# Kernel optimization log

Hardware: AMD Instinct MI355X
Metric: run time of the kernel (lower is better)

## Reference

```python
import jax, jax.numpy as jnp
import numpy as np

B, S, DIM, BITS, HEXPERTS = 4, 4096, 2048, 32, 4


def setup_inputs() -> dict:
    key = jax.random.key(0)
    ks = jax.random.split(key, 6)
    scale = 1.0 / np.sqrt(DIM)
    return {
        "x": jax.random.normal(ks[0], (B, S, DIM), dtype=jnp.float32),
        "A1_w": jax.random.normal(ks[1], (BITS, DIM), dtype=jnp.float32) * scale,
        "A1_b": jax.random.normal(ks[2], (BITS,), dtype=jnp.float32) * 0.01,
        "emb": jax.random.normal(ks[3], (BITS, DIM), dtype=jnp.float32),
        "aggr_w": jax.random.normal(ks[4], (HEXPERTS,), dtype=jnp.float32) * 0.5,
        "aggr_b": jax.random.normal(ks[5], (1,), dtype=jnp.float32) * 0.01,
    }


def reference(x, A1_w, A1_b, emb, aggr_w, aggr_b):
    # Router: small linear [B,S,DIM] -> [B,S,BITS], softmax over bits.
    logits = jnp.einsum("bsd,kd->bsk", x, A1_w) + A1_b
    h_c = jax.nn.softmax(logits, axis=-1)
    # Top-k expert selection (k = Hexperts = 4), sorted descending like torch.topk.
    v, i = jax.lax.top_k(h_c, HEXPERTS)  # v,i: [B,S,4]
    # Gather expert embeddings: [B,S,4,DIM]
    h_emb = emb[i]
    # Scale by gate values and combine across experts with the 4->1 linear.
    # expert_aggr(h_emb.transpose(-2,-1)) == sum_e v[...,e]*h_emb[...,e,:]*w[e] + b
    out = jnp.einsum("bse,bsed,e->bsd", v, h_emb, aggr_w) + aggr_b[0]
    # Residual multiply (dropout p=0 -> identity).
    return x * out
```

## Files before the change

kernel.cpp:

```cpp
#include <hip/hip_runtime.h>


#define NTOK 16384
#define DIMV 2048

__global__ __launch_bounds__(256, 2) void router_k(
    const float* __restrict__ x,
    const float* __restrict__ A1w,
    const float* __restrict__ A1b,
    const float* __restrict__ aggw,
    float* __restrict__ gates)
{
    __shared__ float smem[4608];
    const int tid  = threadIdx.x;
    const int wid  = tid >> 6;
    const int lane = tid & 63;
    const int tg   = lane & 7;
    const int kg   = lane >> 3;
    const int tok0 = blockIdx.x << 5;
    const int d0   = wid << 9;

    float* xs  = smem + wid * 1152;
    float* wsx = xs + 576;

    const int srow = lane >> 2;
    const int scol = (lane & 3) << 2;

    const float* xg0 = x   + (size_t)(tok0 + srow)      * DIMV + d0 + scol;
    const float* xg1 = x   + (size_t)(tok0 + srow + 16) * DIMV + d0 + scol;
    const float* wg0 = A1w + (size_t)(srow)             * DIMV + d0 + scol;
    const float* wg1 = A1w + (size_t)(srow + 16)        * DIMV + d0 + scol;

    float2 acc[4][4];
    #pragma unroll
    for (int i = 0; i < 4; ++i)
        #pragma unroll
        for (int j = 0; j < 4; ++j) acc[i][j] = make_float2(0.f, 0.f);

    float4 px0 = *(const float4*)(xg0);
    float4 px1 = *(const float4*)(xg1);
    float4 pw0 = *(const float4*)(wg0);
    float4 pw1 = *(const float4*)(wg1);

    for (int c = 0; c < 32; ++c) {
        {
            float* a = xs  + srow * 18 + scol;
            float* b = xs  + (srow + 16) * 18 + scol;
            float* d = wsx + srow * 18 + scol;
            float* e = wsx + (srow + 16) * 18 + scol;
            *(float2*)(a)     = make_float2(px0.x, px0.y);
            *(float2*)(a + 2) = make_float2(px0.z, px0.w);
            *(float2*)(b)     = make_float2(px1.x, px1.y);
            *(float2*)(b + 2) = make_float2(px1.z, px1.w);
            *(float2*)(d)     = make_float2(pw0.x, pw0.y);
            *(float2*)(d + 2) = make_float2(pw0.z, pw0.w);
            *(float2*)(e)     = make_float2(pw1.x, pw1.y);
            *(float2*)(e + 2) = make_float2(pw1.z, pw1.w);
        }
        {
            const int cn = (c + 1) & 31;
            px0 = *(const float4*)(xg0 + cn * 16);
            px1 = *(const float4*)(xg1 + cn * 16);
            pw0 = *(const float4*)(wg0 + cn * 16);
            pw1 = *(const float4*)(wg1 + cn * 16);
        }
        #pragma unroll
        for (int dd = 0; dd < 16; dd += 2) {
            float2 xv[4], wv[4];
            #pragma unroll
            for (int i = 0; i < 4; ++i)
                xv[i] = *(const float2*)&xs[(4 * tg + i) * 18 + dd];
            #pragma unroll
            for (int j = 0; j < 4; ++j)
                wv[j] = *(const float2*)&wsx[(4 * kg + j) * 18 + dd];
            #pragma unroll
            for (int i = 0; i < 4; ++i)
                #pragma unroll
                for (int j = 0; j < 4; ++j) {
                    acc[i][j].x = fmaf(xv[i].x, wv[j].x, acc[i][j].x);
                    acc[i][j].y = fmaf(xv[i].y, wv[j].y, acc[i][j].y);
                }
        }
    }

    __syncthreads();
    float* red = smem;
    #pragma unroll
    for (int i = 0; i < 4; ++i)
        #pragma unroll
        for (int j = 0; j < 4; ++j)
            red[(4 * tg + i) * 132 + (4 * kg + j) * 4 + wid] =
                acc[i][j].x + acc[i][j].y;
    __syncthreads();

    if (tid < 32) {
        const int t = tid;
        float l[32];
        #pragma unroll
        for (int k = 0; k < 32; ++k) {
            float4 p = *(const float4*)&red[t * 132 + k * 4];
            l[k] = (p.x + p.y) + (p.z + p.w) + A1b[k];
        }
        float m = l[0];
        #pragma unroll
        for (int k = 1; k < 32; ++k) m = fmaxf(m, l[k]);
        float s = 0.f;
        #pragma unroll
        for (int k = 0; k < 32; ++k) { l[k] = expf(l[k] - m); s += l[k]; }
        const float inv = 1.0f / s;

        unsigned used = 0u;
        float gv[4]; unsigned iv[4];
        #pragma unroll
        for (int e = 0; e < 4; ++e) {
            float best = -1.f; int bi = 0;
            #pragma unroll
            for (int k = 0; k < 32; ++k) {
                bool ok = !((used >> k) & 1u) && (l[k] > best);
                best = ok ? l[k] : best;
                bi   = ok ? k    : bi;
            }
            used |= (1u << bi);
            gv[e] = best * inv * aggw[e];
            iv[e] = (unsigned)bi;
        }
        float* gp = gates + (size_t)(tok0 + t) * 8;
        *(float4*)gp = make_float4(gv[0], gv[1], gv[2], gv[3]);
        *(float4*)(gp + 4) = make_float4(__uint_as_float(iv[0]), __uint_as_float(iv[1]),
                                         __uint_as_float(iv[2]), __uint_as_float(iv[3]));
    }
}

__global__ __launch_bounds__(256) void moe_out_k(
    const float* __restrict__ x,
    const float* __restrict__ emb,
    const float* __restrict__ gates,
    const float* __restrict__ aggb,
    float* __restrict__ out)
{
    const int t   = blockIdx.x;
    const int tid = threadIdx.x;
    const float* gp = gates + (size_t)t * 8;
    const float4 g  = *(const float4*)gp;
    const float4 ibits = *(const float4*)(gp + 4);
    const unsigned i0 = __float_as_uint(ibits.x);
    const unsigned i1 = __float_as_uint(ibits.y);
    const unsigned i2 = __float_as_uint(ibits.z);
    const unsigned i3 = __float_as_uint(ibits.w);
    const float b = aggb[0];
    const size_t base = (size_t)t * DIMV;

    #pragma unroll
    for (int h = 0; h < DIMV; h += 1024) {
        const int d = h + (tid << 2);
        const float4 xv = *(const float4*)&x[base + d];
        const float4 e0 = *(const float4*)&emb[(size_t)i0 * DIMV + d];
        const float4 e1 = *(const float4*)&emb[(size_t)i1 * DIMV + d];
        const float4 e2 = *(const float4*)&emb[(size_t)i2 * DIMV + d];
        const float4 e3 = *(const float4*)&emb[(size_t)i3 * DIMV + d];
        float4 a, o;
        a.x = fmaf(g.x, e0.x, fmaf(g.y, e1.x, fmaf(g.z, e2.x, fmaf(g.w, e3.x, b))));
        a.y = fmaf(g.x, e0.y, fmaf(g.y, e1.y, fmaf(g.z, e2.y, fmaf(g.w, e3.y, b))));
        a.z = fmaf(g.x, e0.z, fmaf(g.y, e1.z, fmaf(g.z, e2.z, fmaf(g.w, e3.z, b))));
        a.w = fmaf(g.x, e0.w, fmaf(g.y, e1.w, fmaf(g.z, e2.w, fmaf(g.w, e3.w, b))));
        o.x = xv.x * a.x; o.y = xv.y * a.y; o.z = xv.z * a.z; o.w = xv.w * a.w;
        *(float4*)&out[base + d] = o;
    }
}

extern "C" void kernel_launch(void* const* d_in, const int* in_sizes, int n_in,
                              void* d_out, int out_size, void* d_ws, size_t ws_size,
                              hipStream_t stream)
{
    (void)in_sizes; (void)n_in; (void)out_size; (void)ws_size;
    const float* x    = (const float*)d_in[0];
    const float* A1w  = (const float*)d_in[1];
    const float* A1b  = (const float*)d_in[2];
    const float* emb  = (const float*)d_in[3];
    const float* aggw = (const float*)d_in[4];
    const float* aggb = (const float*)d_in[5];
    float* out   = (float*)d_out;
    float* gates = (float*)d_ws;

    router_k<<<512, 256, 0, stream>>>(x, A1w, A1b, aggw, gates);
    moe_out_k<<<NTOK, 256, 0, stream>>>(x, emb, gates, aggb, out);
}
```

Baseline: 98.95 us.

## Fuse router and expert-combine kernels into one block-per-32-token kernel

Merges the router GEMM/softmax/top-k kernel and the output kernel into one launch. Each 512-thread block computes gates for 32 tokens, keeps them in LDS, then writes the outputs for those same tokens. This removes the gates round-trip through global memory and the second launch. It also re-reads x soon after first touching it, so the second read may hit L2 or MALL instead of HBM. The cost is that most threads sit idle during the serial 32-thread softmax/top-k phase. There is also only one wave of 512 blocks, which limits latency hiding.

```diff
diff --git a/kernel.cpp b/kernel.cpp
--- a/kernel.cpp
+++ b/kernel.cpp
@@ -4,21 +4,25 @@
 #define NTOK 16384
 #define DIMV 2048
 
-__global__ __launch_bounds__(256, 2) void router_k(
+__global__ __launch_bounds__(512, 4) void fused_moe(
     const float* __restrict__ x,
     const float* __restrict__ A1w,
     const float* __restrict__ A1b,
+    const float* __restrict__ emb,
     const float* __restrict__ aggw,
-    float* __restrict__ gates)
+    const float* __restrict__ aggb,
+    float* __restrict__ out)
 {
-    __shared__ float smem[4608];
+    __shared__ float smem[9216];
+    __shared__ float g_lds[256];
+
     const int tid  = threadIdx.x;
     const int wid  = tid >> 6;
     const int lane = tid & 63;
     const int tg   = lane & 7;
     const int kg   = lane >> 3;
     const int tok0 = blockIdx.x << 5;
-    const int d0   = wid << 9;
+    const int d0   = wid << 8;
 
     float* xs  = smem + wid * 1152;
     float* wsx = xs + 576;
@@ -42,7 +46,7 @@
     float4 pw0 = *(const float4*)(wg0);
     float4 pw1 = *(const float4*)(wg1);
 
-    for (int c = 0; c < 32; ++c) {
+    for (int c = 0; c < 16; ++c) {
         {
             float* a = xs  + srow * 18 + scol;
             float* b = xs  + (srow + 16) * 18 + scol;
@@ -58,7 +62,7 @@
             *(float2*)(e + 2) = make_float2(pw1.z, pw1.w);
         }
         {
-            const int cn = (c + 1) & 31;
+            const int cn = (c + 1) & 15;
             px0 = *(const float4*)(xg0 + cn * 16);
             px1 = *(const float4*)(xg1 + cn * 16);
             pw0 = *(const float4*)(wg0 + cn * 16);
@@ -89,7 +93,7 @@
     for (int i = 0; i < 4; ++i)
         #pragma unroll
         for (int j = 0; j < 4; ++j)
-            red[(4 * tg + i) * 132 + (4 * kg + j) * 4 + wid] =
+            red[(4 * tg + i) * 260 + ((4 * kg + j) << 3) + wid] =
                 acc[i][j].x + acc[i][j].y;
     __syncthreads();
 
@@ -98,8 +102,10 @@
         float l[32];
         #pragma unroll
         for (int k = 0; k < 32; ++k) {
-            float4 p = *(const float4*)&red[t * 132 + k * 4];
-            l[k] = (p.x + p.y) + (p.z + p.w) + A1b[k];
+            float4 p0 = *(const float4*)&red[t * 260 + (k << 3)];
+            float4 p1 = *(const float4*)&red[t * 260 + (k << 3) + 4];
+            l[k] = ((p0.x + p0.y) + (p0.z + p0.w))
+                 + ((p1.x + p1.y) + (p1.z + p1.w)) + A1b[k];
         }
         float m = l[0];
         #pragma unroll
@@ -110,7 +116,6 @@
         const float inv = 1.0f / s;
 
         unsigned used = 0u;
-        float gv[4]; unsigned iv[4];
         #pragma unroll
         for (int e = 0; e < 4; ++e) {
             float best = -1.f; int bi = 0;
@@ -121,48 +126,35 @@
                 bi   = ok ? k    : bi;
             }
             used |= (1u << bi);
-            gv[e] = best * inv * aggw[e];
-            iv[e] = (unsigned)bi;
+            g_lds[t * 8 + e]     = best * inv * aggw[e];
+            g_lds[t * 8 + 4 + e] = __uint_as_float((unsigned)bi);
         }
-        float* gp = gates + (size_t)(tok0 + t) * 8;
-        *(float4*)gp = make_float4(gv[0], gv[1], gv[2], gv[3]);
-        *(float4*)(gp + 4) = make_float4(__uint_as_float(iv[0]), __uint_as_float(iv[1]),
-                                         __uint_as_float(iv[2]), __uint_as_float(iv[3]));
     }
-}
+    __syncthreads();
 
-__global__ __launch_bounds__(256) void moe_out_k(
-    const float* __restrict__ x,
-    const float* __restrict__ emb,
-    const float* __restrict__ gates,
-    const float* __restrict__ aggb,
-    float* __restrict__ out)
-{
-    const int t   = blockIdx.x;
-    const int tid = threadIdx.x;
-    const float* gp = gates + (size_t)t * 8;
-    const float4 g  = *(const float4*)gp;
-    const float4 ibits = *(const float4*)(gp + 4);
-    const unsigned i0 = __float_as_uint(ibits.x);
-    const unsigned i1 = __float_as_uint(ibits.y);
-    const unsigned i2 = __float_as_uint(ibits.z);
-    const unsigned i3 = __float_as_uint(ibits.w);
-    const float b = aggb[0];
-    const size_t base = (size_t)t * DIMV;
+    const int tt  = tid >> 4;
+    const int l16 = tid & 15;
+    const float4 g = *(const float4*)&g_lds[tt * 8];
+    const unsigned i0 = __float_as_uint(g_lds[tt * 8 + 4]);
+    const unsigned i1 = __float_as_uint(g_lds[tt * 8 + 5]);
+    const unsigned i2 = __float_as_uint(g_lds[tt * 8 + 6]);
+    const unsigned i3 = __float_as_uint(g_lds[tt * 8 + 7]);
+    const float bb = aggb[0];
+    const size_t base = (size_t)(tok0 + tt) * DIMV;
 
-    #pragma unroll
-    for (int h = 0; h < DIMV; h += 1024) {
-        const int d = h + (tid << 2);
+    #pragma unroll 4
+    for (int it = 0; it < 32; ++it) {
+        const int d = (l16 << 2) + (it << 6);
         const float4 xv = *(const float4*)&x[base + d];
         const float4 e0 = *(const float4*)&emb[(size_t)i0 * DIMV + d];
         const float4 e1 = *(const float4*)&emb[(size_t)i1 * DIMV + d];
         const float4 e2 = *(const float4*)&emb[(size_t)i2 * DIMV + d];
         const float4 e3 = *(const float4*)&emb[(size_t)i3 * DIMV + d];
         float4 a, o;
-        a.x = fmaf(g.x, e0.x, fmaf(g.y, e1.x, fmaf(g.z, e2.x, fmaf(g.w, e3.x, b))));
-        a.y = fmaf(g.x, e0.y, fmaf(g.y, e1.y, fmaf(g.z, e2.y, fmaf(g.w, e3.y, b))));
-        a.z = fmaf(g.x, e0.z, fmaf(g.y, e1.z, fmaf(g.z, e2.z, fmaf(g.w, e3.z, b))));
-        a.w = fmaf(g.x, e0.w, fmaf(g.y, e1.w, fmaf(g.z, e2.w, fmaf(g.w, e3.w, b))));
+        a.x = fmaf(g.x, e0.x, fmaf(g.y, e1.x, fmaf(g.z, e2.x, fmaf(g.w, e3.x, bb))));
+        a.y = fmaf(g.x, e0.y, fmaf(g.y, e1.y, fmaf(g.z, e2.y, fmaf(g.w, e3.y, bb))));
+        a.z = fmaf(g.x, e0.z, fmaf(g.y, e1.z, fmaf(g.z, e2.z, fmaf(g.w, e3.z, bb))));
+        a.w = fmaf(g.x, e0.w, fmaf(g.y, e1.w, fmaf(g.z, e2.w, fmaf(g.w, e3.w, bb))));
         o.x = xv.x * a.x; o.y = xv.y * a.y; o.z = xv.z * a.z; o.w = xv.w * a.w;
         *(float4*)&out[base + d] = o;
     }
@@ -172,16 +164,14 @@
                               void* d_out, int out_size, void* d_ws, size_t ws_size,
                               hipStream_t stream)
 {
-    (void)in_sizes; (void)n_in; (void)out_size; (void)ws_size;
+    (void)in_sizes; (void)n_in; (void)out_size; (void)d_ws; (void)ws_size;
     const float* x    = (const float*)d_in[0];
     const float* A1w  = (const float*)d_in[1];
     const float* A1b  = (const float*)d_in[2];
     const float* emb  = (const float*)d_in[3];
     const float* aggw = (const float*)d_in[4];
     const float* aggb = (const float*)d_in[5];
-    float* out   = (float*)d_out;
-    float* gates = (float*)d_ws;
+    float* out = (float*)d_out;
 
-    router_k<<<512, 256, 0, stream>>>(x, A1w, A1b, aggw, gates);
-    moe_out_k<<<NTOK, 256, 0, stream>>>(x, emb, gates, aggb, out);
+    fused_moe<<<NTOK / 32, 512, 0, stream>>>(x, A1w, A1b, emb, aggw, aggb, out);
 }
```

After: 107.6 us. +8.8%, slower.

## Restructure router GEMM: per-lane token rows, direct global-to-LDS x loads, weights from cache

Applied to the files above, without the earlier changes.

The router kernel now uses 512-thread blocks over 64 tokens. Each wave owns a 256-wide slice of DIM, and each lane computes all 32 logits for one token. x tiles are streamed into double-buffered LDS with global_load_lds, using a rotated slot layout to avoid bank conflicts. A1_w is read directly from global/L1 as wave-uniform broadcasts instead of being staged in LDS. Partial sums are then reduced across 8 waves through LDS. This is meant to cut LDS traffic and register shuffling, at the cost of more global weight loads and 32 accumulators per lane.

```diff
diff --git a/kernel.cpp b/kernel.cpp
--- a/kernel.cpp
+++ b/kernel.cpp
@@ -4,102 +4,110 @@
 #define NTOK 16384
 #define DIMV 2048
 
-__global__ __launch_bounds__(256, 2) void router_k(
+typedef const __attribute__((address_space(1))) unsigned int* as1_u32p;
+typedef __attribute__((address_space(3))) unsigned int* as3_u32p;
+
+__global__ __launch_bounds__(512, 2) void router_k(
     const float* __restrict__ x,
     const float* __restrict__ A1w,
     const float* __restrict__ A1b,
     const float* __restrict__ aggw,
     float* __restrict__ gates)
 {
-    __shared__ float smem[4608];
+    __shared__ float smem[18944];
+
     const int tid  = threadIdx.x;
-    const int wid  = tid >> 6;
     const int lane = tid & 63;
-    const int tg   = lane & 7;
-    const int kg   = lane >> 3;
-    const int tok0 = blockIdx.x << 5;
-    const int d0   = wid << 9;
+    const int wid  = __builtin_amdgcn_readfirstlane(tid >> 6);
+    const int tok0 = blockIdx.x << 6;
+    const int dbase = wid << 8;
 
-    float* xs  = smem + wid * 1152;
-    float* wsx = xs + 576;
+    float* xw = smem + (wid << 11);
 
     const int srow = lane >> 2;
-    const int scol = (lane & 3) << 2;
+    const int sslot = ((lane & 3) + (lane >> 2)) & 3;
+    const float* xsrc0 = x + (size_t)(tok0 + srow) * DIMV + dbase + (sslot << 2);
 
-    const float* xg0 = x   + (size_t)(tok0 + srow)      * DIMV + d0 + scol;
-    const float* xg1 = x   + (size_t)(tok0 + srow + 16) * DIMV + d0 + scol;
-    const float* wg0 = A1w + (size_t)(srow)             * DIMV + d0 + scol;
-    const float* wg1 = A1w + (size_t)(srow + 16)        * DIMV + d0 + scol;
+    const int rbase = ((lane >> 4) << 8) + ((lane & 15) << 4);
+    int roff[4];
+    #pragma unroll
+    for (int s = 0; s < 4; ++s) roff[s] = rbase + (((s - lane) & 3) << 2);
 
-    float2 acc[4][4];
+    float acc[32];
     #pragma unroll
-    for (int i = 0; i < 4; ++i)
-        #pragma unroll
-        for (int j = 0; j < 4; ++j) acc[i][j] = make_float2(0.f, 0.f);
+    for (int k = 0; k < 32; ++k) acc[k] = 0.f;
 
-    float4 px0 = *(const float4*)(xg0);
-    float4 px1 = *(const float4*)(xg1);
-    float4 pw0 = *(const float4*)(wg0);
-    float4 pw1 = *(const float4*)(wg1);
+    #pragma unroll
+    for (int j = 0; j < 4; ++j)
+        __builtin_amdgcn_global_load_lds(
+            (as1_u32p)(const void*)(xsrc0 + (size_t)(j << 4) * DIMV),
+            (as3_u32p)(void*)(xw + (j << 8)), 16, 0, 0);
+    asm volatile("s_waitcnt vmcnt(0)" ::: "memory");
 
-    for (int c = 0; c < 32; ++c) {
-        {
-            float* a = xs  + srow * 18 + scol;
-            float* b = xs  + (srow + 16) * 18 + scol;
-            float* d = wsx + srow * 18 + scol;
-            float* e = wsx + (srow + 16) * 18 + scol;
-            *(float2*)(a)     = make_float2(px0.x, px0.y);
-            *(float2*)(a + 2) = make_float2(px0.z, px0.w);
-            *(float2*)(b)     = make_float2(px1.x, px1.y);
-            *(float2*)(b + 2) = make_float2(px1.z, px1.w);
-            *(float2*)(d)     = make_float2(pw0.x, pw0.y);
-            *(float2*)(d + 2) = make_float2(pw0.z, pw0.w);
-            *(float2*)(e)     = make_float2(pw1.x, pw1.y);
-            *(float2*)(e + 2) = make_float2(pw1.z, pw1.w);
-        }
-        {
-            const int cn = (c + 1) & 31;
-            px0 = *(const float4*)(xg0 + cn * 16);
-            px1 = *(const float4*)(xg1 + cn * 16);
-            pw0 = *(const float4*)(wg0 + cn * 16);
-            pw1 = *(const float4*)(wg1 + cn * 16);
-        }
-        #pragma unroll
-        for (int dd = 0; dd < 16; dd += 2) {
-            float2 xv[4], wv[4];
-            #pragma unroll
-            for (int i = 0; i < 4; ++i)
-                xv[i] = *(const float2*)&xs[(4 * tg + i) * 18 + dd];
+    int buf = 0;
+    for (int c = 0; c < 16; ++c) {
+        if (c < 15) {
+            const float* src = xsrc0 + ((c + 1) << 4);
+            float* dst = xw + ((buf ^ 1) << 10);
             #pragma unroll
             for (int j = 0; j < 4; ++j)
-                wv[j] = *(const float2*)&wsx[(4 * kg + j) * 18 + dd];
-            #pragma unroll
-            for (int i = 0; i < 4; ++i)
-                #pragma unroll
-                for (int j = 0; j < 4; ++j) {
-                    acc[i][j].x = fmaf(xv[i].x, wv[j].x, acc[i][j].x);
-                    acc[i][j].y = fmaf(xv[i].y, wv[j].y, acc[i][j].y);
-                }
+                __builtin_amdgcn_global_load_lds(
+                    (as1_u32p)(const void*)(src + (size_t)(j << 4) * DIMV),
+                    (as3_u32p)(void*)(dst + (j << 8)), 16, 0, 0);
         }
+        const float* xb = xw + (buf << 10);
+        const float4 x0 = *(const float4*)&xb[roff[0]];
+        const float4 x1 = *(const float4*)&xb[roff[1]];
+        const float4 x2 = *(const float4*)&xb[roff[2]];
+        const float4 x3 = *(const float4*)&xb[roff[3]];
+        const float* wrow = A1w + dbase + (c << 4);
+        #pragma unroll
+        for (int k = 0; k < 32; ++k) {
+            const float4 w0 = *(const float4*)&wrow[k * DIMV];
+            const float4 w1 = *(const float4*)&wrow[k * DIMV + 4];
+            const float4 w2 = *(const float4*)&wrow[k * DIMV + 8];
+            const float4 w3 = *(const float4*)&wrow[k * DIMV + 12];
+            float a = acc[k];
+            a = fmaf(x0.x, w0.x, a); a = fmaf(x0.y, w0.y, a);
+            a = fmaf(x0.z, w0.z, a); a = fmaf(x0.w, w0.w, a);
+            a = fmaf(x1.x, w1.x, a); a = fmaf(x1.y, w1.y, a);
+            a = fmaf(x1.z, w1.z, a); a = fmaf(x1.w, w1.w, a);
+            a = fmaf(x2.x, w2.x, a); a = fmaf(x2.y, w2.y, a);
+            a = fmaf(x2.z, w2.z, a); a = fmaf(x2.w, w2.w, a);
+            a = fmaf(x3.x, w3.x, a); a = fmaf(x3.y, w3.y, a);
+            a = fmaf(x3.z, w3.z, a); a = fmaf(x3.w, w3.w, a);
+            acc[k] = a;
+        }
+        asm volatile("s_waitcnt vmcnt(0)" ::: "memory");
+        buf ^= 1;
     }
 
     __syncthreads();
     float* red = smem;
-    #pragma unroll
-    for (int i = 0; i < 4; ++i)
+    {
+        float* r = red + wid * 2304 + lane * 36;
         #pragma unroll
-        for (int j = 0; j < 4; ++j)
-            red[(4 * tg + i) * 132 + (4 * kg + j) * 4 + wid] =
-                acc[i][j].x + acc[i][j].y;
+        for (int q = 0; q < 8; ++q)
+            *(float4*)&r[q << 2] = make_float4(acc[4*q], acc[4*q+1],
+                                               acc[4*q+2], acc[4*q+3]);
+    }
     __syncthreads();
 
-    if (tid < 32) {
+    if (tid < 64) {
         const int t = tid;
         float l[32];
         #pragma unroll
-        for (int k = 0; k < 32; ++k) {
-            float4 p = *(const float4*)&red[t * 132 + k * 4];
-            l[k] = (p.x + p.y) + (p.z + p.w) + A1b[k];
+        for (int q = 0; q < 8; ++q) {
+            float4 v = make_float4(0.f, 0.f, 0.f, 0.f);
+            #pragma unroll
+            for (int w = 0; w < 8; ++w) {
+                const float4 p = *(const float4*)&red[w * 2304 + t * 36 + (q << 2)];
+                v.x += p.x; v.y += p.y; v.z += p.z; v.w += p.w;
+            }
+            l[4*q]   = v.x + A1b[4*q];
+            l[4*q+1] = v.y + A1b[4*q+1];
+            l[4*q+2] = v.z + A1b[4*q+2];
+            l[4*q+3] = v.w + A1b[4*q+3];
         }
         float m = l[0];
         #pragma unroll
@@ -182,6 +190,6 @@
     float* out   = (float*)d_out;
     float* gates = (float*)d_ws;
 
-    router_k<<<512, 256, 0, stream>>>(x, A1w, A1b, aggw, gates);
+    router_k<<<NTOK / 64, 512, 0, stream>>>(x, A1w, A1b, aggw, gates);
     moe_out_k<<<NTOK, 256, 0, stream>>>(x, emb, gates, aggb, out);
 }
```

Result: slower. 143.5 us (+45.0%).
